# Optimization experiments

Measured on AMD Instinct MI355X. Metric: run time of the kernel, lower is better.

The kernel has to match this reference:

```python
import jax, jax.numpy as jnp
import numpy as np

DIM = 192
HEADS = 6
WIN = (2, 6, 12)          # (pl, lat, lon)
TOW = 64                  # type_of_windows = (8//2)*(96//6)
N_TOK = WIN[0] * WIN[1] * WIN[2]            # 144
TABLE_ROWS = WIN[0]**2 * WIN[1]**2 * (2 * WIN[2] - 1)  # 3312


def calc_position_bias_indices(size):
    pl, la, lo = size
    plq = np.arange(pl); plk = -np.arange(pl) * pl
    laq = np.arange(la); lak = -np.arange(la) * la
    lon = np.arange(lo)
    gq = np.stack(np.meshgrid(plq, laq, lon, indexing='ij'))  # [3,pl,la,lo]
    gk = np.stack(np.meshgrid(plk, lak, lon, indexing='ij'))
    fq = gq.reshape(3, -1)
    fk = gk.reshape(3, -1)
    d = fq[:, :, None] - fk[:, None, :]          # [3,N,N]
    d = np.transpose(d, (1, 2, 0)).copy()
    d[:, :, 2] += lo - 1
    d[:, :, 1] *= 2 * lo - 1
    d[:, :, 0] *= (2 * lo - 1) * la * la
    return d.sum(-1)                              # [N,N]


def setup_inputs() -> dict:
    key = jax.random.key(0)
    ks = jax.random.split(key, 7)
    B_, nW, N, C = 15, TOW, N_TOK, DIM
    x = jax.random.normal(ks[0], (B_, nW, N, C), jnp.float32)
    mask = jax.random.normal(ks[1], (15, nW, N, N), jnp.float32)  # nLon=15
    qkv_w = jax.random.normal(ks[2], (3 * C, C), jnp.float32) * 0.02
    qkv_b = jnp.zeros((3 * C,), jnp.float32)
    table = jax.random.normal(ks[3], (TABLE_ROWS, TOW, HEADS), jnp.float32) * 0.02
    proj_w = jax.random.normal(ks[4], (C, C), jnp.float32) * 0.02
    proj_b = jnp.zeros((C,), jnp.float32)
    pos_index = jnp.asarray(calc_position_bias_indices(WIN), jnp.int32)  # [N,N]
    return {"x": x, "mask": mask, "qkv_w": qkv_w, "qkv_b": qkv_b,
            "table": table, "proj_w": proj_w, "proj_b": proj_b,
            "pos_index": pos_index}


def reference(x, mask, qkv_w, qkv_b, table, proj_w, proj_b, pos_index):
    B_, nW, N, C = x.shape
    h = HEADS
    hd = C // h
    scale = hd ** -0.5
    # qkv projection -> (3, B_, h, nW, N, hd)
    qkv = (jnp.einsum('bwnc,dc->bwnd', x, qkv_w) + qkv_b)
    qkv = qkv.reshape(B_, nW, N, 3, h, hd).transpose(3, 0, 4, 1, 2, 5)
    q, k, v = qkv[0] * scale, qkv[1], qkv[2]
    attn = jnp.einsum('bhwqd,bhwkd->bhwqk', q, k)      # [B_,h,nW,N,N]
    # gather earth position bias: [N,N,tow,h] -> [h,tow,N,N]
    bias = table[pos_index.reshape(-1)].reshape(N, N, nW, h)
    bias = bias.transpose(3, 2, 0, 1)
    attn = attn + bias[None]
    nLon = mask.shape[0]
    attn = attn.reshape(B_ // nLon, nLon, h, nW, N, N) + mask[None, :, None]
    attn = attn.reshape(B_, h, nW, N, N)
    attn = jax.nn.softmax(attn, axis=-1)
    out = jnp.einsum('bhwqk,bhwkd->bhwqd', attn, v)
    out = out.transpose(0, 2, 3, 1, 4).reshape(B_, nW, N, C)
    return jnp.einsum('bwnc,dc->bwnd', out, proj_w) + proj_b
```

## Files before the change

### kernel.cpp

```cpp
#include <hip/hip_runtime.h>

#define HEADS 6
#define N_TOK 144
#define DIM   192
#define NW    64
#define NB    15
#define NBW   (NB * NW)
#define CHUNK 480

typedef __attribute__((ext_vector_type(8))) short bf16x8;
typedef __attribute__((ext_vector_type(4))) float f32x4;

#define MFMA(a, b, c) __builtin_amdgcn_mfma_f32_16x16x32_bf16(a, b, c, 0, 0, 0)

static __device__ __forceinline__ short f2bf(float f) {
    union { float f; unsigned u; } v; v.f = f;
    unsigned r = v.u + 0x7FFFu + ((v.u >> 16) & 1u);
    return (short)(r >> 16);
}
static __device__ __forceinline__ float bf2f(short s) {
    union { unsigned u; float f; } v;
    v.u = ((unsigned)(unsigned short)s) << 16;
    return v.f;
}
static __device__ __forceinline__ unsigned pk2(float a, float b) {
    return (unsigned)(unsigned short)f2bf(a) |
           ((unsigned)(unsigned short)f2bf(b) << 16);
}

__global__ __launch_bounds__(256)
void bias_k(const float* __restrict__ table, const int* __restrict__ pos_index,
            short* __restrict__ bias_bf) {
    const int t = blockIdx.x;
    for (int e = threadIdx.x; e < N_TOK * N_TOK; e += 256) {
        int idx = pos_index[e];
        bias_bf[(long)t * (N_TOK * N_TOK) + e] = f2bf(table[(long)idx * 384 + t]);
    }
}

__global__ __launch_bounds__(256)
void cvt_k(const float* __restrict__ w, short* __restrict__ o, int n) {
    int i = blockIdx.x * 256 + threadIdx.x;
    if (i < n) o[i] = f2bf(w[i]);
}

__global__ __launch_bounds__(256)
void cvtx_k(const float* __restrict__ x, short* __restrict__ xb, int n4) {
    int i = blockIdx.x * 256 + threadIdx.x;
    if (i < n4) {
        float4 f = ((const float4*)x)[i];
        short4 s = { f2bf(f.x), f2bf(f.y), f2bf(f.z), f2bf(f.w) };
        ((short4*)xb)[i] = s;
    }
}

__global__ __launch_bounds__(576)
void qkvs_k(const short* __restrict__ xb, const short* __restrict__ qkvw_bf,
            const float* __restrict__ qkv_b, short* __restrict__ qk_ws,
            short* __restrict__ vT_ws) {
    __shared__ short wlds[192 * 200];

    const int sel = blockIdx.x % 3;
    const int bwL = blockIdx.x / 3;
    const int tid = threadIdx.x;

    for (int u = tid * 8; u < 192 * 192; u += 576 * 8) {
        int r = u / 192, c = u - r * 192;
        *(bf16x8*)&wlds[r * 200 + c] = *(const bf16x8*)&qkvw_bf[sel * 36864 + u];
    }
    __syncthreads();

    const int wid = tid >> 6, lane = tid & 63, lq = lane & 15, lg = lane >> 4;
    const int mg = wid / 3, ng = wid % 3;
    const short* xrow = xb + (long)bwL * N_TOK * DIM;

    f32x4 acc[3][4] = {};
    for (int ks = 0; ks < 6; ++ks) {
        const int k0 = ks * 32 + 8 * lg;
        bf16x8 av[3], bv[4];
        #pragma unroll
        for (int mt = 0; mt < 3; ++mt)
            av[mt] = *(const bf16x8*)&xrow[(mg * 48 + mt * 16 + lq) * DIM + k0];
        #pragma unroll
        for (int nt = 0; nt < 4; ++nt)
            bv[nt] = *(const bf16x8*)&wlds[(ng * 64 + nt * 16 + lq) * 200 + k0];
        #pragma unroll
        for (int mt = 0; mt < 3; ++mt)
            #pragma unroll
            for (int nt = 0; nt < 4; ++nt)
                acc[mt][nt] = MFMA(av[mt], bv[nt], acc[mt][nt]);
    }
    __syncthreads();

    const float scale = 0.17677669529663687f;

    if (sel < 2) {
        #pragma unroll
        for (int nt = 0; nt < 4; ++nt) {
            const int cd = ng * 64 + nt * 16 + lq;
            const float bb = qkv_b[sel * 192 + cd];
            #pragma unroll
            for (int mt = 0; mt < 3; ++mt)
                #pragma unroll
                for (int i = 0; i < 4; ++i) {
                    int row = mg * 48 + mt * 16 + 4 * lg + i;
                    float v = acc[mt][nt][i] + bb;
                    if (sel == 0) v *= scale;
                    wlds[row * 200 + cd] = f2bf(v);
                }
        }
        __syncthreads();
        short* ob = qk_ws + (long)bwL * 6 * 2 * 4608 + (long)sel * 4608;
        #pragma unroll
        for (int j = 0; j < 6; ++j) {
            int u = (j * 576 + tid) * 8;
            int h = u / 4608, rem = u - h * 4608;
            int row = rem >> 5, e = rem & 31;
            *(bf16x8*)&ob[(long)h * 2 * 4608 + rem] =
                *(const bf16x8*)&wlds[row * 200 + h * 32 + e];
        }
    } else {
        #pragma unroll
        for (int nt = 0; nt < 4; ++nt) {
            const int cd = ng * 64 + nt * 16 + lq;
            const float bb = qkv_b[2 * 192 + cd];
            #pragma unroll
            for (int mt = 0; mt < 3; ++mt)
                #pragma unroll
                for (int i = 0; i < 4; ++i) {
                    int row = mg * 48 + mt * 16 + 4 * lg + i;
                    wlds[cd * 152 + row] = f2bf(acc[mt][nt][i] + bb);
                }
        }
        __syncthreads();
        short* ob = vT_ws + (long)bwL * 6 * 4608;
        #pragma unroll
        for (int j = 0; j < 6; ++j) {
            int u = (j * 576 + tid) * 8;
            int h = u / 4608, rem = u - h * 4608;
            int e = rem / 144, row0 = rem - e * 144;
            *(bf16x8*)&ob[(long)h * 4608 + e * 144 + row0] =
                *(const bf16x8*)&wlds[(h * 32 + e) * 152 + row0];
        }
    }
}

__global__ __launch_bounds__(576)
void attn2v_k(const short* __restrict__ qk_ws, const short* __restrict__ vT_ws,
              const short* __restrict__ bias_bf, const float* __restrict__ mask,
              short* __restrict__ tmp, int bw0) {
    __shared__ short vlds[32 * 152];
    __shared__ short pws[9 * 16 * 40];

    const int p = blockIdx.x;
    const int l = (p & 7) * 360 + (p >> 3);
    const int h   = l % HEADS;
    const int bwL = l / HEADS;
    const int bwG = bw0 + bwL;
    const int tid = threadIdx.x;
    const int lane = tid & 63, lq = lane & 15, lg = lane >> 4;
    const int wid = tid >> 6;
    const int m0 = wid * 16;
    const int q  = m0 + lq;
    const int w  = bwG & 63;

    {
        const short* vsrc = vT_ws + (long)(bwL * 6 + h) * 4608;
        int e = tid / 18, k0 = (tid % 18) * 8;
        bf16x8 v = *(const bf16x8*)&vsrc[e * N_TOK + k0];
        *(bf16x8*)&vlds[e * 152 + k0] = v;
    }
    __syncthreads();

    const short* qb = qk_ws + (long)(bwL * 6 + h) * 2 * 4608;
    const short* kb = qb + 4608;

    const f32x4 zf = {};
    bf16x8 bq = *(const bf16x8*)&qb[q * 32 + 8 * lg];
    f32x4 lgt[9];
    #pragma unroll
    for (int nt = 0; nt < 9; ++nt) {
        bf16x8 ak = *(const bf16x8*)&kb[(nt * 16 + lq) * 32 + 8 * lg];
        lgt[nt] = MFMA(ak, bq, zf);
    }

    const short* bp = bias_bf + (long)(w * 6 + h) * (N_TOK * N_TOK)
                    + q * N_TOK + 4 * lg;
    const float* mp = mask + (long)bwG * (N_TOK * N_TOK) + q * N_TOK + 4 * lg;
    #pragma unroll
    for (int nt = 0; nt < 9; ++nt) {
        short4 bs = *(const short4*)&bp[nt * 16];
        float4 mf = *(const float4*)&mp[nt * 16];
        lgt[nt][0] += bf2f(bs.x) + mf.x;
        lgt[nt][1] += bf2f(bs.y) + mf.y;
        lgt[nt][2] += bf2f(bs.z) + mf.z;
        lgt[nt][3] += bf2f(bs.w) + mf.w;
    }

    float m = lgt[0][0];
    #pragma unroll
    for (int nt = 0; nt < 9; ++nt)
        #pragma unroll
        for (int i = 0; i < 4; ++i) m = fmaxf(m, lgt[nt][i]);
    m = fmaxf(m, __shfl_xor(m, 16));
    m = fmaxf(m, __shfl_xor(m, 32));
    float s = 0.f;
    #pragma unroll
    for (int nt = 0; nt < 9; ++nt)
        #pragma unroll
        for (int i = 0; i < 4; ++i) {
            float pe = __expf(lgt[nt][i] - m);
            lgt[nt][i] = pe;
            s += pe;
        }
    s += __shfl_xor(s, 16);
    s += __shfl_xor(s, 32);
    const float inv = 1.f / s;

    short* pw = pws + wid * 16 * 40;
    f32x4 o[2] = {};
    const bf16x8 zb = {};
    #pragma unroll
    for (int kt = 0; kt < 5; ++kt) {
        const int nt0 = 2 * kt;
        *(unsigned*)&pw[lq * 40 + 4 * lg]     = pk2(lgt[nt0][0], lgt[nt0][1]);
        *(unsigned*)&pw[lq * 40 + 4 * lg + 2] = pk2(lgt[nt0][2], lgt[nt0][3]);
        if (kt < 4) {
            const int nt1 = nt0 + 1;
            *(unsigned*)&pw[lq * 40 + 16 + 4 * lg]     = pk2(lgt[nt1][0], lgt[nt1][1]);
            *(unsigned*)&pw[lq * 40 + 16 + 4 * lg + 2] = pk2(lgt[nt1][2], lgt[nt1][3]);
        }
        bf16x8 bpf = *(const bf16x8*)&pw[lq * 40 + 8 * lg];
        #pragma unroll
        for (int et = 0; et < 2; ++et) {
            bf16x8 av = *(const bf16x8*)&vlds[(et * 16 + lq) * 152 + kt * 32 + 8 * lg];
            bf16x8 aa = av, bb = bpf;
            if (kt == 4 && lg >= 2) { aa = zb; bb = zb; }
            o[et] = MFMA(aa, bb, o[et]);
        }
    }

    short* tb = tmp + ((long)bwL * N_TOK + q) * DIM + h * 32;
    #pragma unroll
    for (int et = 0; et < 2; ++et) {
        short4 sx = { f2bf(o[et][0] * inv), f2bf(o[et][1] * inv),
                      f2bf(o[et][2] * inv), f2bf(o[et][3] * inv) };
        *(short4*)&tb[et * 16 + 4 * lg] = sx;
    }
}

__global__ __launch_bounds__(192)
void proj_k(const short* __restrict__ tmp, const short* __restrict__ pwt,
            const float* __restrict__ proj_b, float* __restrict__ out, int bw0) {
    const int bid = blockIdx.x;
    const int mthird = bid % 3;
    const int bwL = bid / 3;
    const int bwG = bw0 + bwL;
    const int tid = threadIdx.x;
    const int wid = tid >> 6, lane = tid & 63, lq = lane & 15, lg = lane >> 4;
    const int m0 = (mthird * 3 + wid) * 16;
    const short* tb = tmp + (long)bwL * N_TOK * DIM;

    f32x4 acc[12] = {};
    for (int ks = 0; ks < 6; ++ks) {
        const int k0 = ks * 32 + 8 * lg;
        bf16x8 a = *(const bf16x8*)&tb[(m0 + lq) * DIM + k0];
        #pragma unroll
        for (int nt = 0; nt < 12; ++nt) {
            bf16x8 b = *(const bf16x8*)&pwt[(nt * 16 + lq) * DIM + k0];
            acc[nt] = MFMA(a, b, acc[nt]);
        }
    }
    float* ob = out + (long)bwG * N_TOK * DIM;
    #pragma unroll
    for (int nt = 0; nt < 12; ++nt) {
        float pb = proj_b[nt * 16 + lq];
        #pragma unroll
        for (int i = 0; i < 4; ++i)
            ob[(m0 + 4 * lg + i) * DIM + nt * 16 + lq] = acc[nt][i] + pb;
    }
}

extern "C" void kernel_launch(void* const* d_in, const int* in_sizes, int n_in,
                              void* d_out, int out_size, void* d_ws, size_t ws_size,
                              hipStream_t stream) {
    const float* x        = (const float*)d_in[0];
    const float* mask     = (const float*)d_in[1];
    const float* qkv_w    = (const float*)d_in[2];
    const float* qkv_b    = (const float*)d_in[3];
    const float* table    = (const float*)d_in[4];
    const float* proj_w   = (const float*)d_in[5];
    const float* proj_b   = (const float*)d_in[6];
    const int*   pos_index= (const int*)d_in[7];
    float* out = (float*)d_out;

    short* bias_bf  = (short*)d_ws;
    short* projw_bf = bias_bf + (size_t)384 * N_TOK * N_TOK;
    short* qkvw_bf  = projw_bf + 36864;
    short* xbf_ws   = qkvw_bf + 110592;
    short* tmp_ws   = xbf_ws;
    short* qk_ws    = xbf_ws + (size_t)CHUNK * N_TOK * DIM;
    short* vT_ws    = qk_ws + (size_t)CHUNK * 6 * 2 * 4608;

    bias_k<<<384, 256, 0, stream>>>(table, pos_index, bias_bf);
    cvt_k<<<144, 256, 0, stream>>>(proj_w, projw_bf, DIM * DIM);
    cvt_k<<<432, 256, 0, stream>>>(qkv_w, qkvw_bf, 3 * DIM * DIM);

    const int n4 = CHUNK * N_TOK * DIM / 4;
    for (int c = 0; c < 2; ++c) {
        const int bw0 = c * CHUNK;
        cvtx_k<<<(n4 + 255) / 256, 256, 0, stream>>>(
            x + (long)bw0 * N_TOK * DIM, xbf_ws, n4);
        qkvs_k<<<CHUNK * 3, 576, 0, stream>>>(xbf_ws, qkvw_bf, qkv_b,
                                              qk_ws, vT_ws);
        attn2v_k<<<CHUNK * 6, 576, 0, stream>>>(qk_ws, vT_ws, bias_bf, mask,
                                                tmp_ws, bw0);
        proj_k<<<CHUNK * 3, 192, 0, stream>>>(tmp_ws, projw_bf, proj_b, out, bw0);
    }
}
```

Before: 445.1 us.

## Split attention into single-wave blocks per 16-row query tile

Replaces the 9-wave attention block, which handled one (window, head) pair and staged V in LDS behind a barrier, with one-wave blocks that each process a single 16-query tile. V is now read directly from global memory, and the block-index swizzle is adjusted for the 9x larger grid. This removes the block-wide barrier and LDS staging so scheduling is finer-grained and occupancy is easier to reach. In exchange, V is re-read from global/L2 by nine blocks instead of once, and the padded final k-tile now reads slightly past each V row in global memory.

```diff
diff --git a/kernel.cpp b/kernel.cpp
--- a/kernel.cpp
+++ b/kernel.cpp
@@ -115,9 +115,8 @@
         for (int j = 0; j < 6; ++j) {
             int u = (j * 576 + tid) * 8;
             int h = u / 4608, rem = u - h * 4608;
-            int row = rem >> 5, e = rem & 31;
             *(bf16x8*)&ob[(long)h * 2 * 4608 + rem] =
-                *(const bf16x8*)&wlds[row * 200 + h * 32 + e];
+                *(const bf16x8*)&wlds[(rem >> 5) * 200 + h * 32 + (rem & 31)];
         }
     } else {
         #pragma unroll
@@ -145,32 +144,21 @@
     }
 }
 
-__global__ __launch_bounds__(576)
-void attn2v_k(const short* __restrict__ qk_ws, const short* __restrict__ vT_ws,
+__global__ __launch_bounds__(64, 4)
+void attn1w_k(const short* __restrict__ qk_ws, const short* __restrict__ vT_ws,
               const short* __restrict__ bias_bf, const float* __restrict__ mask,
               short* __restrict__ tmp, int bw0) {
-    __shared__ short vlds[32 * 152];
-    __shared__ short pws[9 * 16 * 40];
+    __shared__ short pws[16 * 40];
 
     const int p = blockIdx.x;
-    const int l = (p & 7) * 360 + (p >> 3);
-    const int h   = l % HEADS;
-    const int bwL = l / HEADS;
+    const int l = (p & 7) * 3240 + (p >> 3);
+    const int mt9 = l % 9;
+    const int h   = (l / 9) % HEADS;
+    const int bwL = l / 54;
     const int bwG = bw0 + bwL;
-    const int tid = threadIdx.x;
-    const int lane = tid & 63, lq = lane & 15, lg = lane >> 4;
-    const int wid = tid >> 6;
-    const int m0 = wid * 16;
-    const int q  = m0 + lq;
-    const int w  = bwG & 63;
-
-    {
-        const short* vsrc = vT_ws + (long)(bwL * 6 + h) * 4608;
-        int e = tid / 18, k0 = (tid % 18) * 8;
-        bf16x8 v = *(const bf16x8*)&vsrc[e * N_TOK + k0];
-        *(bf16x8*)&vlds[e * 152 + k0] = v;
-    }
-    __syncthreads();
+    const int lane = threadIdx.x & 63, lq = lane & 15, lg = lane >> 4;
+    const int q = mt9 * 16 + lq;
+    const int w = bwG & 63;
 
     const short* qb = qk_ws + (long)(bwL * 6 + h) * 2 * 4608;
     const short* kb = qb + 4608;
@@ -217,23 +205,23 @@
     s += __shfl_xor(s, 32);
     const float inv = 1.f / s;
 
-    short* pw = pws + wid * 16 * 40;
+    const short* vsrc = vT_ws + (long)(bwL * 6 + h) * 4608;
     f32x4 o[2] = {};
     const bf16x8 zb = {};
     #pragma unroll
     for (int kt = 0; kt < 5; ++kt) {
         const int nt0 = 2 * kt;
-        *(unsigned*)&pw[lq * 40 + 4 * lg]     = pk2(lgt[nt0][0], lgt[nt0][1]);
-        *(unsigned*)&pw[lq * 40 + 4 * lg + 2] = pk2(lgt[nt0][2], lgt[nt0][3]);
+        *(unsigned*)&pws[lq * 40 + 4 * lg]     = pk2(lgt[nt0][0], lgt[nt0][1]);
+        *(unsigned*)&pws[lq * 40 + 4 * lg + 2] = pk2(lgt[nt0][2], lgt[nt0][3]);
         if (kt < 4) {
             const int nt1 = nt0 + 1;
-            *(unsigned*)&pw[lq * 40 + 16 + 4 * lg]     = pk2(lgt[nt1][0], lgt[nt1][1]);
-            *(unsigned*)&pw[lq * 40 + 16 + 4 * lg + 2] = pk2(lgt[nt1][2], lgt[nt1][3]);
-        }
-        bf16x8 bpf = *(const bf16x8*)&pw[lq * 40 + 8 * lg];
+            *(unsigned*)&pws[lq * 40 + 16 + 4 * lg]     = pk2(lgt[nt1][0], lgt[nt1][1]);
+            *(unsigned*)&pws[lq * 40 + 16 + 4 * lg + 2] = pk2(lgt[nt1][2], lgt[nt1][3]);
+        }
+        bf16x8 bpf = *(const bf16x8*)&pws[lq * 40 + 8 * lg];
         #pragma unroll
         for (int et = 0; et < 2; ++et) {
-            bf16x8 av = *(const bf16x8*)&vlds[(et * 16 + lq) * 152 + kt * 32 + 8 * lg];
+            bf16x8 av = *(const bf16x8*)&vsrc[(et * 16 + lq) * N_TOK + kt * 32 + 8 * lg];
             bf16x8 aa = av, bb = bpf;
             if (kt == 4 && lg >= 2) { aa = zb; bb = zb; }
             o[et] = MFMA(aa, bb, o[et]);
@@ -313,7 +301,7 @@
             x + (long)bw0 * N_TOK * DIM, xbf_ws, n4);
         qkvs_k<<<CHUNK * 3, 576, 0, stream>>>(xbf_ws, qkvw_bf, qkv_b,
                                               qk_ws, vT_ws);
-        attn2v_k<<<CHUNK * 6, 576, 0, stream>>>(qk_ws, vT_ws, bias_bf, mask,
+        attn1w_k<<<CHUNK * 54, 64, 0, stream>>>(qk_ws, vT_ws, bias_bf, mask,
                                                 tmp_ws, bw0);
         proj_k<<<CHUNK * 3, 192, 0, stream>>>(tmp_ws, projw_bf, proj_b, out, bw0);
     }
```

Result: slower. 460.2 us (+3.4%).
